# Performance work log

Hardware: AMD Instinct MI355X
Metric: run time of the kernel (lower is better)

Reference implementation:

```python
import jax, jax.numpy as jnp
import numpy as np

B, N, D_MODEL, N_HEADS, WINDOW = 2, 2048, 1024, 16, 512
HEAD_DIM = D_MODEL // N_HEADS

def setup_inputs() -> dict:
    key = jax.random.key(0)
    k1, k2, k3 = jax.random.split(key, 3)
    x = jax.random.normal(k1, (B, N, D_MODEL), dtype=jnp.float32)
    W_qkv = jax.random.normal(k2, (D_MODEL, 3 * D_MODEL), dtype=jnp.float32) * 0.02
    W_proj = jax.random.normal(k3, (D_MODEL, D_MODEL), dtype=jnp.float32) * 0.02
    b_proj = jnp.zeros((D_MODEL,), dtype=jnp.float32)
    return {"x": x, "W_qkv": W_qkv, "W_proj": W_proj, "b_proj": b_proj}

def reference(x, W_qkv, W_proj, b_proj):
    Bx, Nx, C = x.shape
    H, Dh = N_HEADS, C // N_HEADS
    scale = Dh ** -0.5
    window = min(WINDOW, Nx)
    half = window // 2
    # qkv: [B,N,3C] -> [3,B,H,N,Dh]
    qkv = (x @ W_qkv).reshape(Bx, Nx, 3, H, Dh).transpose(2, 0, 3, 1, 4)
    q, k, v = qkv[0], qkv[1], qkv[2]
    # banded mask: allowed iff i-half <= j <= i+half
    i = jnp.arange(Nx)[:, None]
    j = jnp.arange(Nx)[None, :]
    allowed = jnp.abs(i - j) <= half  # [N,N] bool
    attn = jnp.einsum('bhqd,bhkd->bhqk', q, k) * scale
    attn = jnp.where(allowed[None, None], attn, -jnp.inf)
    attn = jax.nn.softmax(attn, axis=-1)
    out = jnp.einsum('bhqk,bhkd->bhqd', attn, v)
    out = out.transpose(0, 2, 1, 3).reshape(Bx, Nx, C)
    return out @ W_proj + b_proj
```

## Files before the change

kernel.cpp:

```cpp
#include <hip/hip_runtime.h>
#include <stdint.h>


typedef _Float16 f16x8 __attribute__((ext_vector_type(8)));
typedef _Float16 f16x4 __attribute__((ext_vector_type(4)));
typedef __fp16   fp16x2n __attribute__((ext_vector_type(2)));
typedef float    f32x2 __attribute__((ext_vector_type(2)));
typedef float    f32x4 __attribute__((ext_vector_type(4)));
typedef float    f32x16 __attribute__((ext_vector_type(16)));

#define MFMA16(a, b, c) __builtin_amdgcn_mfma_f32_16x16x32_f16((a), (b), (c), 0, 0, 0)
#define MFMA32(a, b, c) __builtin_amdgcn_mfma_f32_32x32x16_f16((a), (b), (c), 0, 0, 0)

__device__ __forceinline__ void gload16(const void* g, void* l) {
  __builtin_amdgcn_global_load_lds(
      (const __attribute__((address_space(1))) void*)g,
      (__attribute__((address_space(3))) void*)l, 16, 0, 0);
}

__device__ __forceinline__ unsigned pk2(float a, float b) {
  fp16x2n t = __builtin_amdgcn_cvt_pkrtz(a, b);
  return __builtin_bit_cast(unsigned, t);
}

__global__ __launch_bounds__(256) void prep(const float* __restrict__ x,
                                            const float* __restrict__ wqkv,
                                            const float* __restrict__ wproj,
                                            _Float16* __restrict__ Xb,
                                            _Float16* __restrict__ Wqt,
                                            _Float16* __restrict__ Wpt) {
  __shared__ float t[64][65];
  const int id = blockIdx.x, tid = threadIdx.x;
  if (id < 4096) {
    int i = (id * 256 + tid) * 4;
    float4 v = *(const float4*)(x + i);
    f16x4 h;
    h[0] = (_Float16)v.x; h[1] = (_Float16)v.y;
    h[2] = (_Float16)v.z; h[3] = (_Float16)v.w;
    *(f16x4*)(Xb + i) = h;
    return;
  }
  const float* in; _Float16* out; int N, bx, by;
  if (id < 4864) { int tt = id - 4096; in = wqkv; out = Wqt; N = 3072; bx = tt % 48; by = tt / 48; }
  else           { int tt = id - 4864; in = wproj; out = Wpt; N = 1024; bx = tt & 15; by = tt >> 4; }
  const int n0 = bx * 64, k0 = by * 64;
  {
    int j = tid & 63;
#pragma unroll
    for (int p = 0; p < 16; p++) {
      int i = p * 4 + (tid >> 6);
      t[i][j] = in[(size_t)(k0 + i) * N + n0 + j];
    }
  }
  __syncthreads();
  {
    int i = tid & 63;
#pragma unroll
    for (int p = 0; p < 16; p++) {
      int j = p * 4 + (tid >> 6);
      out[(size_t)(n0 + j) * 1024 + k0 + i] = (_Float16)t[i][j];
    }
  }
}

__global__ __launch_bounds__(512) void gemm8p(const _Float16* __restrict__ A,
                                              const _Float16* __restrict__ Bt,
                                              _Float16* __restrict__ oh,
                                              _Float16* __restrict__ vt) {
  __shared__ __align__(16) char smem[147456];
  const int tid = threadIdx.x, wave = tid >> 6, lane = tid & 63;
  const int il = lane & 15, ih = lane >> 4;
  const int rs = lane >> 3, cp = lane & 7;
  const int bm = blockIdx.y * 256, bn = blockIdx.x * 192;
  const int wm = wave >> 2, wn = wave & 3;
  const int srow = wave * 8 + rs;

#define R15_STAGE_A(ABUF, T)                                                  \
  _Pragma("unroll") for (int hh = 0; hh < 4; hh++) {                          \
    int row = hh * 64 + srow;                                                 \
    int c = cp ^ (row & 7);                                                   \
    gload16(A + (size_t)(bm + row) * 1024 + (T) * 64 + c * 8,                 \
            smem + (ABUF) * 32768 + hh * 8192 + wave * 1024);                 \
  }
#define R15_STAGE_B(BBUF, T)                                                  \
  _Pragma("unroll") for (int hh = 0; hh < 3; hh++) {                          \
    int row = hh * 64 + srow;                                                 \
    int c = cp ^ (row & 7);                                                   \
    gload16(Bt + (size_t)(bn + row) * 1024 + (T) * 64 + c * 8,                \
            smem + 98304 + (BBUF) * 24576 + hh * 8192 + wave * 1024);         \
  }

  f32x4 acc[8][3] = {};

  R15_STAGE_A(0, 0);
  R15_STAGE_B(0, 0);
  R15_STAGE_A(1, 1);
  R15_STAGE_B(1, 1);
  asm volatile("s_waitcnt vmcnt(7)" ::: "memory");
  __builtin_amdgcn_s_barrier();

  int ta = 0, sa = 2;
#pragma unroll 1
  for (int t = 0; t < 16; t++) {
    const char* Abuf = (const char*)smem + ta * 32768;
    const char* Bbuf = (const char*)smem + 98304 + (t & 1) * 24576;
    f16x8 af[4][2], ag[4][2], bf[3][2];
#pragma unroll
    for (int m = 0; m < 4; m++) {
      int R = wm * 128 + m * 16 + il;
#pragma unroll
      for (int ks = 0; ks < 2; ks++)
        af[m][ks] = *(const f16x8*)(Abuf + R * 128 + (((ks * 4 + ih) ^ (R & 7)) * 16));
    }
#pragma unroll
    for (int n = 0; n < 3; n++) {
      int C = wn * 48 + n * 16 + il;
#pragma unroll
      for (int ks = 0; ks < 2; ks++)
        bf[n][ks] = *(const f16x8*)(Bbuf + C * 128 + (((ks * 4 + ih) ^ (C & 7)) * 16));
    }
    if (t < 14) { R15_STAGE_A(sa, t + 2); }
    asm volatile("s_waitcnt lgkmcnt(0)" ::: "memory");
    __builtin_amdgcn_s_barrier();
    __builtin_amdgcn_s_setprio(1);
#pragma unroll
    for (int m = 0; m < 4; m++)
#pragma unroll
      for (int n = 0; n < 3; n++)
#pragma unroll
        for (int ks = 0; ks < 2; ks++)
          acc[m][n] = MFMA16(af[m][ks], bf[n][ks], acc[m][n]);
    __builtin_amdgcn_s_setprio(0);
#pragma unroll
    for (int m = 0; m < 4; m++) {
      int R = wm * 128 + 64 + m * 16 + il;
#pragma unroll
      for (int ks = 0; ks < 2; ks++)
        ag[m][ks] = *(const f16x8*)(Abuf + R * 128 + (((ks * 4 + ih) ^ (R & 7)) * 16));
    }
    if (t < 14) { R15_STAGE_B(t & 1, t + 2); }
    __builtin_amdgcn_s_setprio(1);
#pragma unroll
    for (int m = 0; m < 4; m++)
#pragma unroll
      for (int n = 0; n < 3; n++)
#pragma unroll
        for (int ks = 0; ks < 2; ks++)
          acc[4 + m][n] = MFMA16(ag[m][ks], bf[n][ks], acc[4 + m][n]);
    __builtin_amdgcn_s_setprio(0);
    if (t <= 13) {
      asm volatile("s_waitcnt vmcnt(7)" ::: "memory");
    } else if (t == 14) {
      asm volatile("s_waitcnt vmcnt(0)" ::: "memory");
    }
    if (t < 15) __builtin_amdgcn_s_barrier();
    ta = (ta == 2) ? 0 : ta + 1;
    sa = (sa == 2) ? 0 : sa + 1;
  }

#pragma unroll
  for (int mi = 0; mi < 8; mi++)
#pragma unroll
    for (int ni = 0; ni < 3; ni++) {
      int row0 = bm + wm * 128 + mi * 16 + ih * 4;
      int col = bn + wn * 48 + ni * 16 + il;
      int sec = col >> 10, cc = col & 1023;
      if (sec == 2) {
        int b = row0 >> 11, n = row0 & 2047;
        int bh2 = b * 16 + (cc >> 6), dh = cc & 63;
        union { f16x4 h; uint2 u; } pk;
#pragma unroll
        for (int r = 0; r < 4; r++) pk.h[r] = (_Float16)acc[mi][ni][r];
        *(uint2*)(vt + (size_t)bh2 * 131072 + (size_t)dh * 2048 + n) = pk.u;
      } else {
#pragma unroll
        for (int r = 0; r < 4; r++) {
          int row = row0 + r;
          float v = acc[mi][ni][r];
          if (sec == 0) v *= 0.18033688f;
          size_t plane = (size_t)(sec * 32 + (row >> 11) * 16 + (cc >> 6));
          oh[plane * 131072 + (size_t)(row & 2047) * 64 + (cc & 63)] = (_Float16)v;
        }
      }
    }
#undef R15_STAGE_A
#undef R15_STAGE_B
}

template <int BM, int BN, int EPI>
__global__ __launch_bounds__(256) void gemm16(const _Float16* __restrict__ A,
                                              const _Float16* __restrict__ Bt,
                                              const int K,
                                              _Float16* __restrict__ oh,
                                              _Float16* __restrict__ vt,
                                              float* __restrict__ of,
                                              const float* __restrict__ bias,
                                              const int Nout) {
  constexpr int RF = BM / 32, CF = BN / 32;
  constexpr int SLABS = (BM + BN) / 8;
  __shared__ __align__(16) char smem[(BM + BN) * 128];
  char* As = smem;
  char* Bs = smem + BM * 128;
  const int tid = threadIdx.x, wave = tid >> 6, lane = tid & 63;
  const int il = lane & 15, ih = lane >> 4;
  const int bm = blockIdx.y * BM, bn = blockIdx.x * BN;
  const int wm = wave >> 1, wn = wave & 1;
  const int rs = lane >> 3, cp = lane & 7;

  f32x4 acc[RF][CF] = {};

  for (int k0 = 0; k0 < K; k0 += 64) {
    __syncthreads();
#pragma unroll
    for (int s0 = 0; s0 < SLABS / 4; s0++) {
      int s = wave + s0 * 4;
      int row = s * 8 + rs;
      int c = cp ^ (row & 7);
      if (row < BM)
        gload16(A + (size_t)(bm + row) * K + k0 + c * 8, As + s * 1024);
      else
        gload16(Bt + (size_t)(bn + row - BM) * K + k0 + c * 8, smem + s * 1024);
    }
    __syncthreads();
#pragma unroll
    for (int ks = 0; ks < 2; ks++) {
      f16x8 af[RF], bf[CF];
#pragma unroll
      for (int rf = 0; rf < RF; rf++) {
        int R = wm * (BM / 2) + rf * 16 + il;
        af[rf] = *(const f16x8*)(As + R * 128 + (((ks * 4 + ih) ^ (R & 7)) * 16));
      }
#pragma unroll
      for (int cf = 0; cf < CF; cf++) {
        int C = wn * (BN / 2) + cf * 16 + il;
        bf[cf] = *(const f16x8*)(Bs + C * 128 + (((ks * 4 + ih) ^ (C & 7)) * 16));
      }
#pragma unroll
      for (int rf = 0; rf < RF; rf++)
#pragma unroll
        for (int cf = 0; cf < CF; cf++)
          acc[rf][cf] = MFMA16(af[rf], bf[cf], acc[rf][cf]);
    }
  }

#pragma unroll
  for (int rf = 0; rf < RF; rf++)
#pragma unroll
    for (int cf = 0; cf < CF; cf++) {
      int row0 = bm + wm * (BM / 2) + rf * 16 + ih * 4;
      int col = bn + wn * (BN / 2) + cf * 16 + il;
      if (EPI == 0) {
        int sec = col >> 10, cc = col & 1023;
        if (sec == 2) {
          int b = row0 >> 11, n = row0 & 2047;
          int bh = b * 16 + (cc >> 6), dh = cc & 63;
          union { f16x4 h; uint2 u; } pk;
#pragma unroll
          for (int r = 0; r < 4; r++) pk.h[r] = (_Float16)acc[rf][cf][r];
          *(uint2*)(vt + (size_t)bh * 131072 + (size_t)dh * 2048 + n) = pk.u;
        } else {
#pragma unroll
          for (int r = 0; r < 4; r++) {
            int row = row0 + r;
            float v = acc[rf][cf][r];
            if (sec == 0) v *= 0.18033688f;
            size_t plane = (size_t)(sec * 32 + (row >> 11) * 16 + (cc >> 6));
            oh[plane * 131072 + (size_t)(row & 2047) * 64 + (cc & 63)] = (_Float16)v;
          }
        }
      } else {
#pragma unroll
        for (int r = 0; r < 4; r++)
          of[(size_t)(row0 + r) * Nout + col] = acc[rf][cf][r] + bias[col];
      }
    }
}

__global__ __launch_bounds__(512) void attn(const _Float16* __restrict__ QKV,
                                            const _Float16* __restrict__ VT,
                                            _Float16* __restrict__ O2) {
  __shared__ __align__(16) char smem[51200];
  const int tid = threadIdx.x, wave = tid >> 6, lane = tid & 63;
  const int qw = wave >> 1, sh = wave & 1;
  const int cl = lane & 31, hl = lane >> 5;
  const int rs = lane >> 3, cp = lane & 7;
  const int q0 = blockIdx.x * 128, bh = blockIdx.y;
  const _Float16* Qg = QKV + (size_t)bh * 131072;
  const _Float16* Kg = QKV + 4194304 + (size_t)bh * 131072;
  const _Float16* Vg = VT + (size_t)bh * 131072;
  const int t0 = (q0 >= 256) ? q0 - 256 : 0;
  const int t1 = (q0 + 384 <= 2048) ? q0 + 384 : 2048;
  const int niter = (t1 - t0) >> 6;

#pragma unroll
  for (int q = 0; q < 2; q++) {
    int s = 2 * wave + q;
    int row = s * 8 + rs;
    int c = cp ^ (row & 7);
    gload16(Qg + (size_t)(q0 + row) * 64 + c * 8, smem + s * 1024);
  }
  {
    char* B0 = smem + 18432;
    int row = wave * 8 + rs;
    int c = cp ^ (row & 7);
    gload16(Kg + (size_t)(t0 + row) * 64 + c * 8, B0 + wave * 1024);
    gload16(Vg + (size_t)row * 2048 + t0 + c * 8, B0 + 8192 + wave * 1024);
  }
  __syncthreads();

  f16x8 bq[4];
  {
    int row = 32 * qw + cl;
#pragma unroll
    for (int ks = 0; ks < 4; ks++)
      bq[ks] = *(const f16x8*)(smem + row * 128 + (((ks * 2 + hl) ^ (row & 7)) * 16));
  }

  f32x16 oacc[2] = {};
  float l_acc = 0.f;
  const int a0 = q0 + 32 * qw;

  for (int i = 0; i < niter; i++) {
    const int kt = t0 + i * 64;
    char* Bc = smem + 18432 + (i & 1) * 16384;
    if (i + 1 < niter) {
      char* Bn = smem + 18432 + ((i + 1) & 1) * 16384;
      int row = wave * 8 + rs;
      int c = cp ^ (row & 7);
      gload16(Kg + (size_t)(kt + 64 + row) * 64 + c * 8, Bn + wave * 1024);
      gload16(Vg + (size_t)row * 2048 + (kt + 64) + c * 8, Bn + 8192 + wave * 1024);
    }
    const int d0 = a0 - (kt + 32 * sh);
    if (d0 < 288 && d0 > -288) {
      char* Ksm = Bc;
      char* Vsm = Bc + 8192;
      f32x16 st = {};
      {
        const int krow = 32 * sh + cl;
        __builtin_amdgcn_s_setprio(1);
#pragma unroll
        for (int ks = 0; ks < 4; ks++) {
          f16x8 ak = *(const f16x8*)(Ksm + krow * 128 + (((ks * 2 + hl) ^ (krow & 7)) * 16));
          st = MFMA32(ak, bq[ks], st);
        }
        __builtin_amdgcn_s_setprio(0);
      }
      unsigned w0a[4], w1a[4];
#pragma unroll
      for (int g = 0; g < 4; g++) {
        float v[4];
#pragma unroll
        for (int i2 = 0; i2 < 4; i2++) {
          float e = __builtin_amdgcn_exp2f(st[4 * g + i2]);
          int kl = 8 * g + 4 * hl + i2;
          if (d0 == 256) e = (cl <= kl) ? e : 0.f;
          else if (d0 == -256) e = (cl >= kl) ? e : 0.f;
          l_acc += e;
          v[i2] = e;
        }
        w0a[g] = pk2(v[0], v[1]);
        w1a[g] = pk2(v[2], v[3]);
      }
#pragma unroll
      for (int ks2 = 0; ks2 < 2; ks2++) {
        unsigned kA0 = w0a[2 * ks2],     kA1 = w1a[2 * ks2];
        unsigned kB0 = w0a[2 * ks2 + 1], kB1 = w1a[2 * ks2 + 1];
        unsigned keep0 = hl ? kB0 : kA0, keep1 = hl ? kB1 : kA1;
        unsigned send0 = hl ? kA0 : kB0, send1 = hl ? kA1 : kB1;
        unsigned r0 = (unsigned)__shfl_xor((int)send0, 32);
        unsigned r1 = (unsigned)__shfl_xor((int)send1, 32);
        union { unsigned u[4]; f16x8 h; } bp;
        bp.u[0] = hl ? r0 : keep0;
        bp.u[1] = hl ? r1 : keep1;
        bp.u[2] = hl ? keep0 : r0;
        bp.u[3] = hl ? keep1 : r1;
        __builtin_amdgcn_s_setprio(1);
#pragma unroll
        for (int db = 0; db < 2; db++) {
          int vrow = 32 * db + cl;
          f16x8 av = *(const f16x8*)(Vsm + vrow * 128 +
                                     (((4 * sh + 2 * ks2 + hl) ^ (vrow & 7)) * 16));
          oacc[db] = MFMA32(av, bp.h, oacc[db]);
        }
        __builtin_amdgcn_s_setprio(0);
      }
    }
    __syncthreads();
  }

  const float lp = l_acc + __shfl_xor(l_acc, 32);
  char* Mq = smem + qw * 8448;
  if (sh == 1) {
#pragma unroll
    for (int db = 0; db < 2; db++)
#pragma unroll
      for (int g = 0; g < 4; g++) {
        int dh0 = 32 * db + 8 * g + 4 * hl;
        f32x2 a = {oacc[db][4 * g + 0], oacc[db][4 * g + 1]};
        f32x2 b = {oacc[db][4 * g + 2], oacc[db][4 * g + 3]};
        *(f32x2*)(Mq + cl * 264 + dh0 * 4) = a;
        *(f32x2*)(Mq + cl * 264 + dh0 * 4 + 8) = b;
      }
    if (hl == 0) *(float*)(smem + 34816 + (qw * 32 + cl) * 4) = lp;
  }
  __syncthreads();
  if (sh == 0) {
    float lo = *(const float*)(smem + 34816 + (qw * 32 + cl) * 4);
    float inv = 1.0f / (lp + lo);
    const int b = bh >> 4, h = bh & 15;
    _Float16* dst = O2 + (size_t)(b * 2048 + a0 + cl) * 1024 + h * 64;
#pragma unroll
    for (int db = 0; db < 2; db++)
#pragma unroll
      for (int g = 0; g < 4; g++) {
        int dh0 = 32 * db + 8 * g + 4 * hl;
        f32x2 a = *(const f32x2*)(Mq + cl * 264 + dh0 * 4);
        f32x2 b2 = *(const f32x2*)(Mq + cl * 264 + dh0 * 4 + 8);
        uint2 pkd = {pk2((oacc[db][4 * g + 0] + a[0]) * inv,
                         (oacc[db][4 * g + 1] + a[1]) * inv),
                     pk2((oacc[db][4 * g + 2] + b2[0]) * inv,
                         (oacc[db][4 * g + 3] + b2[1]) * inv)};
        *(uint2*)(dst + dh0) = pkd;
      }
  }
}


extern "C" void kernel_launch(void* const* d_in, const int* in_sizes, int n_in,
                              void* d_out, int out_size, void* d_ws, size_t ws_size,
                              hipStream_t stream) {
  const float* x = (const float*)d_in[0];
  const float* wqkv = (const float*)d_in[1];
  const float* wproj = (const float*)d_in[2];
  const float* bproj = (const float*)d_in[3];
  float* out = (float*)d_out;
  char* ws = (char*)d_ws;

  _Float16* Xb  = (_Float16*)(ws);
  _Float16* Wqt = (_Float16*)(ws + (size_t)(8  << 20));
  _Float16* Wpt = (_Float16*)(ws + (size_t)(14 << 20));
  _Float16* QKV = (_Float16*)(ws + (size_t)(16 << 20));
  _Float16* Vt  = (_Float16*)(ws + (size_t)(40 << 20));
  _Float16* O2  = (_Float16*)(ws);

  prep<<<5120, 256, 0, stream>>>(x, wqkv, wproj, Xb, Wqt, Wpt);
  gemm8p<<<dim3(16, 16), 512, 0, stream>>>(Xb, Wqt, QKV, Vt);
  attn<<<dim3(16, 32), 512, 0, stream>>>(QKV, Vt, O2);
  gemm16<128, 64, 1><<<dim3(16, 32), 256, 0, stream>>>(O2, Wpt, 1024, nullptr,
                                                       nullptr, out, bproj, 1024);
}
```

Before: 153.2 us.

## Replace output-projection GEMM with pipelined 128x128 multi-buffered kernel

```diff
diff --git a/kernel.cpp b/kernel.cpp
--- a/kernel.cpp
+++ b/kernel.cpp
@@ -187,93 +187,97 @@
 #undef R15_STAGE_B
 }
 
-template <int BM, int BN, int EPI>
-__global__ __launch_bounds__(256) void gemm16(const _Float16* __restrict__ A,
+__global__ __launch_bounds__(512) void gemm2p(const _Float16* __restrict__ A,
                                               const _Float16* __restrict__ Bt,
-                                              const int K,
-                                              _Float16* __restrict__ oh,
-                                              _Float16* __restrict__ vt,
                                               float* __restrict__ of,
-                                              const float* __restrict__ bias,
-                                              const int Nout) {
-  constexpr int RF = BM / 32, CF = BN / 32;
-  constexpr int SLABS = (BM + BN) / 8;
-  __shared__ __align__(16) char smem[(BM + BN) * 128];
-  char* As = smem;
-  char* Bs = smem + BM * 128;
+                                              const float* __restrict__ bias) {
+  __shared__ __align__(16) char smem[81920];
   const int tid = threadIdx.x, wave = tid >> 6, lane = tid & 63;
   const int il = lane & 15, ih = lane >> 4;
-  const int bm = blockIdx.y * BM, bn = blockIdx.x * BN;
-  const int wm = wave >> 1, wn = wave & 1;
   const int rs = lane >> 3, cp = lane & 7;
-
-  f32x4 acc[RF][CF] = {};
-
-  for (int k0 = 0; k0 < K; k0 += 64) {
-    __syncthreads();
-#pragma unroll
-    for (int s0 = 0; s0 < SLABS / 4; s0++) {
-      int s = wave + s0 * 4;
-      int row = s * 8 + rs;
-      int c = cp ^ (row & 7);
-      if (row < BM)
-        gload16(A + (size_t)(bm + row) * K + k0 + c * 8, As + s * 1024);
-      else
-        gload16(Bt + (size_t)(bn + row - BM) * K + k0 + c * 8, smem + s * 1024);
-    }
-    __syncthreads();
-#pragma unroll
-    for (int ks = 0; ks < 2; ks++) {
-      f16x8 af[RF], bf[CF];
-#pragma unroll
-      for (int rf = 0; rf < RF; rf++) {
-        int R = wm * (BM / 2) + rf * 16 + il;
-        af[rf] = *(const f16x8*)(As + R * 128 + (((ks * 4 + ih) ^ (R & 7)) * 16));
-      }
-#pragma unroll
-      for (int cf = 0; cf < CF; cf++) {
-        int C = wn * (BN / 2) + cf * 16 + il;
-        bf[cf] = *(const f16x8*)(Bs + C * 128 + (((ks * 4 + ih) ^ (C & 7)) * 16));
-      }
-#pragma unroll
-      for (int rf = 0; rf < RF; rf++)
-#pragma unroll
-        for (int cf = 0; cf < CF; cf++)
-          acc[rf][cf] = MFMA16(af[rf], bf[cf], acc[rf][cf]);
-    }
-  }
-
-#pragma unroll
-  for (int rf = 0; rf < RF; rf++)
-#pragma unroll
-    for (int cf = 0; cf < CF; cf++) {
-      int row0 = bm + wm * (BM / 2) + rf * 16 + ih * 4;
-      int col = bn + wn * (BN / 2) + cf * 16 + il;
-      if (EPI == 0) {
-        int sec = col >> 10, cc = col & 1023;
-        if (sec == 2) {
-          int b = row0 >> 11, n = row0 & 2047;
-          int bh = b * 16 + (cc >> 6), dh = cc & 63;
-          union { f16x4 h; uint2 u; } pk;
-#pragma unroll
-          for (int r = 0; r < 4; r++) pk.h[r] = (_Float16)acc[rf][cf][r];
-          *(uint2*)(vt + (size_t)bh * 131072 + (size_t)dh * 2048 + n) = pk.u;
-        } else {
-#pragma unroll
-          for (int r = 0; r < 4; r++) {
-            int row = row0 + r;
-            float v = acc[rf][cf][r];
-            if (sec == 0) v *= 0.18033688f;
-            size_t plane = (size_t)(sec * 32 + (row >> 11) * 16 + (cc >> 6));
-            oh[plane * 131072 + (size_t)(row & 2047) * 64 + (cc & 63)] = (_Float16)v;
-          }
-        }
-      } else {
-#pragma unroll
-        for (int r = 0; r < 4; r++)
-          of[(size_t)(row0 + r) * Nout + col] = acc[rf][cf][r] + bias[col];
-      }
-    }
+  const int bm = blockIdx.y * 128, bn = blockIdx.x * 128;
+  const int wm = wave >> 2, wn = wave & 3;
+  const int srow = wave * 8 + rs;
+
+#define R17_STAGE_A(ABUF, T)                                                  \
+  _Pragma("unroll") for (int hh = 0; hh < 2; hh++) {                          \
+    int row = hh * 64 + srow;                                                 \
+    int c = cp ^ (row & 7);                                                   \
+    gload16(A + (size_t)(bm + row) * 1024 + (T) * 64 + c * 8,                 \
+            smem + (ABUF) * 16384 + hh * 8192 + wave * 1024);                 \
+  }
+#define R17_STAGE_B(BBUF, T)                                                  \
+  _Pragma("unroll") for (int hh = 0; hh < 2; hh++) {                          \
+    int row = hh * 64 + srow;                                                 \
+    int c = cp ^ (row & 7);                                                   \
+    gload16(Bt + (size_t)(bn + row) * 1024 + (T) * 64 + c * 8,                \
+            smem + 49152 + (BBUF) * 16384 + hh * 8192 + wave * 1024);         \
+  }
+
+  f32x4 acc[4][2] = {};
+
+  R17_STAGE_A(0, 0);
+  R17_STAGE_B(0, 0);
+  R17_STAGE_A(1, 1);
+  R17_STAGE_B(1, 1);
+  asm volatile("s_waitcnt vmcnt(4)" ::: "memory");
+  __builtin_amdgcn_s_barrier();
+
+  int ta = 0, sa = 2;
+#pragma unroll 1
+  for (int t = 0; t < 16; t++) {
+    const char* Abuf = (const char*)smem + ta * 16384;
+    const char* Bbuf = (const char*)smem + 49152 + (t & 1) * 16384;
+    f16x8 af[4][2], bf[2][2];
+#pragma unroll
+    for (int m = 0; m < 4; m++) {
+      int R = wm * 64 + m * 16 + il;
+#pragma unroll
+      for (int ks = 0; ks < 2; ks++)
+        af[m][ks] = *(const f16x8*)(Abuf + R * 128 + (((ks * 4 + ih) ^ (R & 7)) * 16));
+    }
+#pragma unroll
+    for (int n = 0; n < 2; n++) {
+      int C = wn * 32 + n * 16 + il;
+#pragma unroll
+      for (int ks = 0; ks < 2; ks++)
+        bf[n][ks] = *(const f16x8*)(Bbuf + C * 128 + (((ks * 4 + ih) ^ (C & 7)) * 16));
+    }
+    if (t < 14) { R17_STAGE_A(sa, t + 2); }
+    asm volatile("s_waitcnt lgkmcnt(0)" ::: "memory");
+    __builtin_amdgcn_s_barrier();
+    if (t < 14) { R17_STAGE_B(t & 1, t + 2); }
+    __builtin_amdgcn_s_setprio(1);
+#pragma unroll
+    for (int m = 0; m < 4; m++)
+#pragma unroll
+      for (int n = 0; n < 2; n++)
+#pragma unroll
+        for (int ks = 0; ks < 2; ks++)
+          acc[m][n] = MFMA16(af[m][ks], bf[n][ks], acc[m][n]);
+    __builtin_amdgcn_s_setprio(0);
+    if (t <= 13) {
+      asm volatile("s_waitcnt vmcnt(4)" ::: "memory");
+    } else if (t == 14) {
+      asm volatile("s_waitcnt vmcnt(0)" ::: "memory");
+    }
+    if (t < 15) __builtin_amdgcn_s_barrier();
+    ta = (ta == 2) ? 0 : ta + 1;
+    sa = (sa == 2) ? 0 : sa + 1;
+  }
+
+#pragma unroll
+  for (int mi = 0; mi < 4; mi++)
+#pragma unroll
+    for (int ni = 0; ni < 2; ni++) {
+      int row0 = bm + wm * 64 + mi * 16 + ih * 4;
+      int col = bn + wn * 32 + ni * 16 + il;
+#pragma unroll
+      for (int r = 0; r < 4; r++)
+        of[(size_t)(row0 + r) * 1024 + col] = acc[mi][ni][r] + bias[col];
+    }
+#undef R17_STAGE_A
+#undef R17_STAGE_B
 }
 
 __global__ __launch_bounds__(512) void attn(const _Float16* __restrict__ QKV,
@@ -446,6 +450,5 @@
   prep<<<5120, 256, 0, stream>>>(x, wqkv, wproj, Xb, Wqt, Wpt);
   gemm8p<<<dim3(16, 16), 512, 0, stream>>>(Xb, Wqt, QKV, Vt);
   attn<<<dim3(16, 32), 512, 0, stream>>>(QKV, Vt, O2);
-  gemm16<128, 64, 1><<<dim3(16, 32), 256, 0, stream>>>(O2, Wpt, 1024, nullptr,
-                                                       nullptr, out, bproj, 1024);
-}
+  gemm2p<<<dim3(8, 32), 512, 0, stream>>>(O2, Wpt, out, bproj);
+}
```

Result: no change. 154.3 us, median of 2 (+0.7%).
